# Kernel optimization log

Measured on AMD Instinct MI355X. Metric: run time of the kernel, lower is better.

The kernel has to match this reference:

```python
import jax, jax.numpy as jnp
import numpy as np

B, S = 128, 200
Q, K, V, C, SUM = 20000, 128, 128, 64, 128


def setup_inputs() -> dict:
    key = jax.random.key(0)
    ks = jax.random.split(key, 14)
    stdev = 1.0 / np.sqrt(C + K)  # NTM-style memory init bound

    def lin_w(k, fan_in, shape):
        b = 1.0 / np.sqrt(fan_in)
        return jax.random.uniform(k, shape, jnp.float32, -b, b)

    # embeddings with padding_idx=0 zeroed (PAD_INDEX=0)
    q_emb = jax.random.normal(ks[0], (Q + 1, K), jnp.float32).at[0].set(0.0)
    i_emb = jax.random.normal(ks[1], (2 * Q + 1, V), jnp.float32).at[0].set(0.0)
    key_memory = jax.random.uniform(ks[2], (K, C), jnp.float32, -stdev, stdev)
    init_value_memory = jax.random.uniform(ks[3], (V, C), jnp.float32, -stdev, stdev)
    erase_W = lin_w(ks[4], V, (V, V))
    erase_b = lin_w(ks[5], V, (V,))
    add_W = lin_w(ks[6], V, (V, V))
    add_b = lin_w(ks[7], V, (V,))
    summ_W = lin_w(ks[8], V + K, (V + K, SUM))
    summ_b = lin_w(ks[9], V + K, (SUM,))
    out_W = lin_w(ks[10], SUM, (SUM, 1))
    out_b = lin_w(ks[11], SUM, (1,))
    inp = jax.random.randint(ks[12], (B, S), 0, 2 * Q + 1)
    target_id = jax.random.randint(ks[13], (B,), 0, Q + 1)
    return dict(q_emb=q_emb, i_emb=i_emb, key_memory=key_memory,
                init_value_memory=init_value_memory,
                erase_W=erase_W, erase_b=erase_b, add_W=add_W, add_b=add_b,
                summ_W=summ_W, summ_b=summ_b, out_W=out_W, out_b=out_b,
                input=inp, target_id=target_id)


def reference(q_emb, i_emb, key_memory, init_value_memory,
              erase_W, erase_b, add_W, add_b,
              summ_W, summ_b, out_W, out_b,
              input, target_id):
    Qn = q_emb.shape[0] - 1
    bsz = input.shape[0]
    # map interaction index -> question id
    qid = input - Qn * (input > Qn).astype(input.dtype)          # (B,S)
    # all per-step quantities are independent of memory state -> precompute
    iv = i_emb[input]                                            # (B,S,V)
    e = jax.nn.sigmoid(iv @ erase_W + erase_b)                   # (B,S,V)
    a = jnp.tanh(iv @ add_W + add_b)                             # (B,S,V)
    w = jax.nn.softmax(q_emb[qid] @ key_memory, axis=-1)         # (B,S,C)

    mem0 = jnp.broadcast_to(init_value_memory, (bsz,) + init_value_memory.shape)  # (B,V,C)

    def step(mem, xs):
        e_t, a_t, w_t = xs                                       # (B,V),(B,V),(B,C)
        erase = e_t[:, :, None] * w_t[:, None, :]                # rank-1 outer, (B,V,C)
        add = a_t[:, :, None] * w_t[:, None, :]
        mem = mem * (1.0 - erase) + add
        return mem, None

    xs = (jnp.swapaxes(e, 0, 1), jnp.swapaxes(a, 0, 1), jnp.swapaxes(w, 0, 1))
    mem, _ = jax.lax.scan(step, mem0, xs)                        # (B,V,C)

    qv = q_emb[target_id]                                        # (B,K)
    wt = jax.nn.softmax(qv @ key_memory, axis=-1)                # (B,C)
    read = jnp.einsum('bvc,bc->bv', mem, wt)                     # (B,V)
    summ = jnp.tanh(jnp.concatenate([read, qv], axis=-1) @ summ_W + summ_b)
    return summ @ out_W + out_b                                  # (B,1), pre-sigmoid
```

## Files before the change

kernel.cpp:

```cpp
#include <hip/hip_runtime.h>
#include <hip/hip_bf16.h>
#include <hip/hip_fp16.h>

#define B_ 128
#define S_ 200
#define QN_ 20000
#define V_ 128
#define K_ 128
#define C_ 64
#define SUM_ 128
#define NCH 8
#define CL 25
#define RW 32

using short8 = __attribute__((ext_vector_type(8))) short;
using f32x4  = __attribute__((ext_vector_type(4))) float;

__device__ __forceinline__ float fast_sigmoid(float x) { return 1.f / (1.f + __expf(-x)); }
__device__ __forceinline__ float fast_tanh(float x)    { return 1.f - 2.f / (__expf(2.f * x) + 1.f); }

template<bool BF>
__device__ __forceinline__ float ld(const void* p, long long i) {
    if (BF) return __bfloat162float(((const __hip_bfloat16*)p)[i]);
    return ((const float*)p)[i];
}

__device__ __forceinline__ unsigned short f2bf(float v) {
    __hip_bfloat16 h = __float2bfloat16(v);
    unsigned short u;
    __builtin_memcpy(&u, &h, 2);
    return u;
}

__device__ __forceinline__ int probe_flag_wave(const void* erase_b) {
    const unsigned* w = (const unsigned*)erase_b;
    const int lane = threadIdx.x & 63;
    const unsigned lo = w[lane] & 0xffffu;
    const float f = __uint_as_float(lo << 16);
    const unsigned long long bal = __ballot(!(fabsf(f) <= 0.5f));
    return (__popcll(bal) <= 8) ? 1 : 0;
}

struct FusedLDS {
    unsigned short bufA[RW * 136];
    unsigned short bufB[RW * 136];
    float  wlog[RW * 68];
    int sidx[RW], sqid[RW];
};

template<bool BF>
__device__ __forceinline__ void fused_body(
    const void* q_emb, const void* i_emb,
    const void* erase_W, const void* add_W, const void* key_memory,
    const void* erase_b, const void* add_b,
    const int* __restrict__ input,
    __half* __restrict__ du, FusedLDS& sm)
{
    const int bid = blockIdx.x;
    const int b = bid & 127;
    const int chunk = bid >> 7;
    const int t = threadIdx.x;
    const int wv = t >> 6;
    const int lane = t & 63;
    const int lrow = lane & 15;
    const int lk8 = (lane >> 4) * 8;

    if (t < RW) {
        const int s = (t < CL) ? t : 0;
        const int ix = input[b * S_ + chunk * CL + s];
        sm.sidx[t] = ix;
        sm.sqid[t] = ix > QN_ ? ix - QN_ : ix;
    }
    __syncthreads();

    #pragma unroll
    for (int r = 0; r < 4; ++r) {
        const int j = t + 256 * r;
        const int tensor = j >> 9;
        const int row = (j >> 4) & 31;
        const int seg = j & 15;
        const int gr = tensor ? sm.sqid[row] : sm.sidx[row];
        unsigned short* dst = (tensor ? sm.bufB : sm.bufA) + row * 136 + seg * 8;
        if (BF) {
            const unsigned short* src = (const unsigned short*)(tensor ? q_emb : i_emb);
            *(uint4*)dst = *(const uint4*)(src + (long long)gr * 128 + seg * 8);
        } else {
            const float* src = (const float*)(tensor ? q_emb : i_emb) + (long long)gr * 128 + seg * 8;
            const float4 f0 = *(const float4*)src;
            const float4 f1 = *(const float4*)(src + 4);
            unsigned short o[8] = {f2bf(f0.x), f2bf(f0.y), f2bf(f0.z), f2bf(f0.w),
                                   f2bf(f1.x), f2bf(f1.y), f2bf(f1.z), f2bf(f1.w)};
            *(uint4*)dst = *(const uint4*)o;
        }
    }

    short8 bfr[5][4];
    int nco[5];
    float biasq[4];
    #pragma unroll
    for (int q = 0; q < 5; ++q) {
        const int nt = wv + 4 * q;
        const void* Wsrc;
        int ldn;
        if (q < 2)      { Wsrc = erase_W;    nco[q] = nt * 16 + lrow;        ldn = 128; }
        else if (q < 4) { Wsrc = add_W;      nco[q] = (nt - 8) * 16 + lrow;  ldn = 128; }
        else            { Wsrc = key_memory; nco[q] = (nt - 16) * 16 + lrow; ldn = 64; }
        if (q < 2)      biasq[q] = ld<BF>(erase_b, nco[q]);
        else if (q < 4) biasq[q] = ld<BF>(add_b, nco[q]);
        #pragma unroll
        for (int ks = 0; ks < 4; ++ks) {
            unsigned short o[8];
            #pragma unroll
            for (int jj = 0; jj < 8; ++jj) {
                const long long idx = (long long)(ks * 32 + lk8 + jj) * ldn + nco[q];
                o[jj] = f2bf(ld<BF>(Wsrc, idx));
            }
            bfr[q][ks] = *(const short8*)o;
        }
    }
    __syncthreads();

    __half* eshw = (__half*)sm.bufA;
    __half* ashw = (__half*)sm.bufB;
    #pragma unroll
    for (int mt = 0; mt < 2; ++mt) {
        short8 afr_iv[4], afr_qv[4];
        const unsigned short* arA = sm.bufA + (mt * 16 + lrow) * 136 + lk8;
        const unsigned short* arB = sm.bufB + (mt * 16 + lrow) * 136 + lk8;
        #pragma unroll
        for (int ks = 0; ks < 4; ++ks) {
            afr_iv[ks] = *(const short8*)(arA + ks * 32);
            afr_qv[ks] = *(const short8*)(arB + ks * 32);
        }
        __syncthreads();
        #pragma unroll
        for (int q = 0; q < 4; ++q) {
            f32x4 acc = {0.f, 0.f, 0.f, 0.f};
            #pragma unroll
            for (int ks = 0; ks < 4; ++ks)
                acc = __builtin_amdgcn_mfma_f32_16x16x32_bf16(afr_iv[ks], bfr[q][ks], acc, 0, 0, 0);
            const int ncol = nco[q];
            const float bb = biasq[q];
            #pragma unroll
            for (int r = 0; r < 4; ++r) {
                const int orow = mt * 16 + (lane >> 4) * 4 + r;
                const float y = acc[r] + bb;
                if (q < 2) eshw[orow * 136 + ncol] = __float2half(fast_sigmoid(y));
                else       ashw[orow * 136 + ncol] = __float2half(fast_tanh(y));
            }
        }
        {
            f32x4 acc = {0.f, 0.f, 0.f, 0.f};
            #pragma unroll
            for (int ks = 0; ks < 4; ++ks)
                acc = __builtin_amdgcn_mfma_f32_16x16x32_bf16(afr_qv[ks], bfr[4][ks], acc, 0, 0, 0);
            #pragma unroll
            for (int r = 0; r < 4; ++r)
                sm.wlog[(mt * 16 + (lane >> 4) * 4 + r) * 68 + nco[4]] = acc[r];
        }
    }
    __syncthreads();

    {
        const int row = t >> 3;
        const int cs = t & 7;
        float* wr = &sm.wlog[row * 68 + cs * 8];
        float v[8];
        *(float4*)&v[0] = *(const float4*)&wr[0];
        *(float4*)&v[4] = *(const float4*)&wr[4];
        float m = v[0];
        #pragma unroll
        for (int ii = 1; ii < 8; ++ii) m = fmaxf(m, v[ii]);
        m = fmaxf(m, __shfl_xor(m, 1, 64));
        m = fmaxf(m, __shfl_xor(m, 2, 64));
        m = fmaxf(m, __shfl_xor(m, 4, 64));
        float s = 0.f;
        #pragma unroll
        for (int ii = 0; ii < 8; ++ii) { v[ii] = __expf(v[ii] - m); s += v[ii]; }
        s += __shfl_xor(s, 1, 64);
        s += __shfl_xor(s, 2, 64);
        s += __shfl_xor(s, 4, 64);
        const float inv = 1.f / s;
        *(float4*)&wr[0] = make_float4(v[0]*inv, v[1]*inv, v[2]*inv, v[3]*inv);
        *(float4*)&wr[4] = make_float4(v[4]*inv, v[5]*inv, v[6]*inv, v[7]*inv);
    }
    __syncthreads();

    const int vg = t >> 3;
    const int cg = t & 7;
    const int v0 = vg * 4, c0 = cg * 8;
    const __half* esh = (const __half*)sm.bufA;
    const __half* ash = (const __half*)sm.bufB;

    const __half2 one2 = __floats2half2_rn(1.f, 1.f);
    const __half2 zero2 = __floats2half2_rn(0.f, 0.f);
    __half2 Dm2[4][4], Um2[4][4];
    #pragma unroll
    for (int i = 0; i < 4; ++i)
        #pragma unroll
        for (int jp = 0; jp < 4; ++jp) { Dm2[i][jp] = one2; Um2[i][jp] = zero2; }

    for (int s = 0; s < CL; ++s) {
        const __half2 e01 = *(const __half2*)(esh + s * 136 + v0);
        const __half2 e23 = *(const __half2*)(esh + s * 136 + v0 + 2);
        const __half2 a01 = *(const __half2*)(ash + s * 136 + v0);
        const __half2 a23 = *(const __half2*)(ash + s * 136 + v0 + 2);
        const float4 wf0 = *(const float4*)(sm.wlog + s * 68 + c0);
        const float4 wf1 = *(const float4*)(sm.wlog + s * 68 + c0 + 4);
        const __half2 w2[4] = { __floats2half2_rn(wf0.x, wf0.y), __floats2half2_rn(wf0.z, wf0.w),
                                __floats2half2_rn(wf1.x, wf1.y), __floats2half2_rn(wf1.z, wf1.w) };
        const __half2 e2[4] = { __low2half2(e01), __high2half2(e01),
                                __low2half2(e23), __high2half2(e23) };
        const __half2 a2[4] = { __low2half2(a01), __high2half2(a01),
                                __low2half2(a23), __high2half2(a23) };
        #pragma unroll
        for (int i = 0; i < 4; ++i) {
            const __half2 ne = __hneg2(e2[i]);
            #pragma unroll
            for (int jp = 0; jp < 4; ++jp) {
                const __half2 d2 = __hfma2(ne, w2[jp], one2);
                Dm2[i][jp] = __hmul2(Dm2[i][jp], d2);
                Um2[i][jp] = __hfma2(d2, Um2[i][jp], __hmul2(a2[i], w2[jp]));
            }
        }
    }

    __half* dbase = du + ((size_t)(chunk * B_ + b) * (V_ * C_ * 2));
    #pragma unroll
    for (int i = 0; i < 4; ++i) {
        __half* dst = dbase + (size_t)(v0 + i) * (C_ * 2) + c0;
        *(uint4*)dst        = *(const uint4*)&Dm2[i][0];
        *(uint4*)(dst + C_) = *(const uint4*)&Um2[i][0];
    }
}

__global__ __launch_bounds__(256) void dkvmn_fused(
    const void* q_emb, const void* i_emb,
    const void* erase_W, const void* add_W, const void* key_memory,
    const void* erase_b, const void* add_b,
    const int* __restrict__ input,
    __half* __restrict__ du)
{
    __shared__ FusedLDS sm;
    if (probe_flag_wave(erase_b))
        fused_body<true>(q_emb, i_emb, erase_W, add_W, key_memory,
                         erase_b, add_b, input, du, sm);
    else
        fused_body<false>(q_emb, i_emb, erase_W, add_W, key_memory,
                          erase_b, add_b, input, du, sm);
}

template<bool BF>
__device__ __forceinline__ void foldfinal_body(
    const void* init_value_memory, const void* q_emb, const void* key_memory,
    const void* summ_W, const void* summ_b,
    const void* out_W, const void* out_b,
    const int* __restrict__ target_id,
    const __half* __restrict__ du,
    void* __restrict__ outp, float* wtl, float* readl, float* summl)
{
    const int b = blockIdx.x;
    const int t = threadIdx.x;
    const int cg = t & 7;
    const int c0 = cg * 8;

    if (t < 64) {
        const long long qrow = (long long)target_id[b] * K_;
        float logit = 0.f;
        #pragma unroll 8
        for (int i = 0; i < K_; ++i)
            logit += ld<BF>(q_emb, qrow + i) * ld<BF>(key_memory, i * C_ + t);
        float m = logit;
        for (int off = 32; off > 0; off >>= 1)
            m = fmaxf(m, __shfl_xor(m, off, 64));
        const float ex = __expf(logit - m);
        float ssum = ex;
        for (int off = 32; off > 0; off >>= 1)
            ssum += __shfl_xor(ssum, off, 64);
        wtl[t] = ex / ssum;
    }
    __syncthreads();

    float wt8[8];
    *(float4*)&wt8[0] = *(const float4*)(wtl + c0);
    *(float4*)&wt8[4] = *(const float4*)(wtl + c0 + 4);

    #pragma unroll
    for (int sub = 0; sub < 4; ++sub) {
        const int v = sub * 32 + (t >> 3);

        uint4 qa[NCH], qb[NCH];
        #pragma unroll
        for (int ch = 0; ch < NCH; ++ch) {
            const __half* base = du + ((size_t)(ch * B_ + b) * (V_ * C_ * 2))
                                    + (size_t)v * (C_ * 2) + c0;
            qa[ch] = *(const uint4*)base;
            qb[ch] = *(const uint4*)(base + C_);
        }

        float mem[8];
        #pragma unroll
        for (int k = 0; k < 8; ++k)
            mem[k] = ld<BF>(init_value_memory, v * C_ + c0 + k);

        #pragma unroll
        for (int ch = 0; ch < NCH; ++ch) {
            const __half2* hD = (const __half2*)&qa[ch];
            const __half2* hU = (const __half2*)&qb[ch];
            #pragma unroll
            for (int k = 0; k < 4; ++k) {
                const float2 fD = __half22float2(hD[k]);
                const float2 fU = __half22float2(hU[k]);
                mem[2 * k]     = fmaf(fD.x, mem[2 * k],     fU.x);
                mem[2 * k + 1] = fmaf(fD.y, mem[2 * k + 1], fU.y);
            }
        }

        float pacc = 0.f;
        #pragma unroll
        for (int k = 0; k < 8; ++k) pacc += mem[k] * wt8[k];
        pacc += __shfl_xor(pacc, 1, 64);
        pacc += __shfl_xor(pacc, 2, 64);
        pacc += __shfl_xor(pacc, 4, 64);
        if (cg == 0) readl[v] = pacc;
    }
    __syncthreads();

    if (t < SUM_) {
        const long long qrow = (long long)target_id[b] * K_;
        float acc = ld<BF>(summ_b, t);
        #pragma unroll 8
        for (int i = 0; i < 128; ++i)
            acc += readl[i] * ld<BF>(summ_W, i * SUM_ + t);
        #pragma unroll 8
        for (int i = 0; i < 128; ++i)
            acc += ld<BF>(q_emb, qrow + i) * ld<BF>(summ_W, (128 + i) * SUM_ + t);
        summl[t] = fast_tanh(acc);
    }
    __syncthreads();

    if (t < 64) {
        float oacc = summl[t] * ld<BF>(out_W, t) + summl[t + 64] * ld<BF>(out_W, t + 64);
        for (int off = 32; off > 0; off >>= 1)
            oacc += __shfl_xor(oacc, off, 64);
        if (t == 0) {
            const float res = oacc + ld<BF>(out_b, 0);
            if (BF) ((__hip_bfloat16*)outp)[b] = __float2bfloat16(res);
            else    ((float*)outp)[b] = res;
        }
    }
}

__global__ __launch_bounds__(256) void dkvmn_foldfinal(
    const void* init_value_memory, const void* q_emb, const void* key_memory,
    const void* summ_W, const void* summ_b,
    const void* out_W, const void* out_b, const void* erase_b,
    const int* __restrict__ target_id,
    const __half* __restrict__ du,
    void* __restrict__ outp)
{
    __shared__ float wtl[C_], readl[V_], summl[SUM_];
    if (probe_flag_wave(erase_b))
        foldfinal_body<true>(init_value_memory, q_emb, key_memory, summ_W, summ_b,
                             out_W, out_b, target_id, du, outp, wtl, readl, summl);
    else
        foldfinal_body<false>(init_value_memory, q_emb, key_memory, summ_W, summ_b,
                              out_W, out_b, target_id, du, outp, wtl, readl, summl);
}

extern "C" void kernel_launch(void* const* d_in, const int* in_sizes, int n_in,
                              void* d_out, int out_size, void* d_ws, size_t ws_size,
                              hipStream_t stream) {
    const void* q_emb             = d_in[0];
    const void* i_emb             = d_in[1];
    const void* key_memory        = d_in[2];
    const void* init_value_memory = d_in[3];
    const void* erase_W           = d_in[4];
    const void* erase_b           = d_in[5];
    const void* add_W             = d_in[6];
    const void* add_b             = d_in[7];
    const void* summ_W            = d_in[8];
    const void* summ_b            = d_in[9];
    const void* out_W             = d_in[10];
    const void* out_b             = d_in[11];
    const int* input     = (const int*)d_in[12];
    const int* target_id = (const int*)d_in[13];

    __half* du = (__half*)d_ws;

    dkvmn_fused<<<NCH * B_, 256, 0, stream>>>(
        q_emb, i_emb, erase_W, add_W, key_memory, erase_b, add_b, input, du);
    dkvmn_foldfinal<<<B_, 256, 0, stream>>>(
        init_value_memory, q_emb, key_memory, summ_W, summ_b, out_W, out_b,
        erase_b, target_id, du, d_out);
}
```

Baseline: 166.4 us.

## Prepack bf16 MFMA weight fragments in a separate kernel and read them directly

Adds a small prepack kernel that converts erase_W, add_W and key_memory into bf16 MFMA B-fragment layout once per call, stored in workspace. The fused kernel no longer gathers scattered strided weight elements and converts them in each of the 1024 blocks. It instead loads contiguous 16-byte fragments at MFMA time, which frees the 20 short8 registers per thread that held the fragments. It also adds a launch_bounds occupancy hint of 4 blocks per CU. The cost is an extra kernel launch and repeated global/L2 reads of the packed weights inside the MFMA loop.

```diff
diff --git a/kernel.cpp b/kernel.cpp
--- a/kernel.cpp
+++ b/kernel.cpp
@@ -41,6 +41,41 @@
     return (__popcll(bal) <= 8) ? 1 : 0;
 }
 
+template<bool BF>
+__device__ __forceinline__ void prepack_body(
+    const void* erase_W, const void* add_W, const void* key_memory,
+    unsigned short* __restrict__ wpack)
+{
+    const int fid = blockIdx.x * 256 + threadIdx.x;
+    if (fid >= 5120) return;
+    const int lane = fid & 63;
+    const int ks = (fid >> 6) & 3;
+    const int wv = (fid >> 8) & 3;
+    const int q  = fid >> 10;
+    const int nt = wv + 4 * q;
+    const void* Wsrc;
+    int ncol, ldn;
+    if (q < 2)      { Wsrc = erase_W;    ncol = nt * 16 + (lane & 15);        ldn = 128; }
+    else if (q < 4) { Wsrc = add_W;      ncol = (nt - 8) * 16 + (lane & 15);  ldn = 128; }
+    else            { Wsrc = key_memory; ncol = (nt - 16) * 16 + (lane & 15); ldn = 64; }
+    const int k8 = (lane >> 4) * 8;
+    unsigned short o[8];
+    #pragma unroll
+    for (int jj = 0; jj < 8; ++jj) {
+        const long long idx = (long long)(ks * 32 + k8 + jj) * ldn + ncol;
+        o[jj] = f2bf(ld<BF>(Wsrc, idx));
+    }
+    *(uint4*)(wpack + (size_t)fid * 8) = *(const uint4*)o;
+}
+
+__global__ __launch_bounds__(256) void dkvmn_prepack(
+    const void* erase_W, const void* add_W, const void* key_memory,
+    const void* erase_b, unsigned short* __restrict__ wpack)
+{
+    if (probe_flag_wave(erase_b)) prepack_body<true >(erase_W, add_W, key_memory, wpack);
+    else                          prepack_body<false>(erase_W, add_W, key_memory, wpack);
+}
+
 struct FusedLDS {
     unsigned short bufA[RW * 136];
     unsigned short bufB[RW * 136];
@@ -51,9 +86,9 @@
 template<bool BF>
 __device__ __forceinline__ void fused_body(
     const void* q_emb, const void* i_emb,
-    const void* erase_W, const void* add_W, const void* key_memory,
     const void* erase_b, const void* add_b,
     const int* __restrict__ input,
+    const unsigned short* __restrict__ wpack,
     __half* __restrict__ du, FusedLDS& sm)
 {
     const int bid = blockIdx.x;
@@ -94,29 +129,16 @@
         }
     }
 
-    short8 bfr[5][4];
     int nco[5];
     float biasq[4];
     #pragma unroll
     for (int q = 0; q < 5; ++q) {
         const int nt = wv + 4 * q;
-        const void* Wsrc;
-        int ldn;
-        if (q < 2)      { Wsrc = erase_W;    nco[q] = nt * 16 + lrow;        ldn = 128; }
-        else if (q < 4) { Wsrc = add_W;      nco[q] = (nt - 8) * 16 + lrow;  ldn = 128; }
-        else            { Wsrc = key_memory; nco[q] = (nt - 16) * 16 + lrow; ldn = 64; }
+        if (q < 2)      nco[q] = nt * 16 + lrow;
+        else if (q < 4) nco[q] = (nt - 8) * 16 + lrow;
+        else            nco[q] = (nt - 16) * 16 + lrow;
         if (q < 2)      biasq[q] = ld<BF>(erase_b, nco[q]);
         else if (q < 4) biasq[q] = ld<BF>(add_b, nco[q]);
-        #pragma unroll
-        for (int ks = 0; ks < 4; ++ks) {
-            unsigned short o[8];
-            #pragma unroll
-            for (int jj = 0; jj < 8; ++jj) {
-                const long long idx = (long long)(ks * 32 + lk8 + jj) * ldn + nco[q];
-                o[jj] = f2bf(ld<BF>(Wsrc, idx));
-            }
-            bfr[q][ks] = *(const short8*)o;
-        }
     }
     __syncthreads();
 
@@ -137,8 +159,11 @@
         for (int q = 0; q < 4; ++q) {
             f32x4 acc = {0.f, 0.f, 0.f, 0.f};
             #pragma unroll
-            for (int ks = 0; ks < 4; ++ks)
-                acc = __builtin_amdgcn_mfma_f32_16x16x32_bf16(afr_iv[ks], bfr[q][ks], acc, 0, 0, 0);
+            for (int ks = 0; ks < 4; ++ks) {
+                const short8 bf = *(const short8*)(wpack +
+                    ((size_t)(((q * 4 + wv) * 4 + ks) * 64 + lane)) * 8);
+                acc = __builtin_amdgcn_mfma_f32_16x16x32_bf16(afr_iv[ks], bf, acc, 0, 0, 0);
+            }
             const int ncol = nco[q];
             const float bb = biasq[q];
             #pragma unroll
@@ -152,8 +177,11 @@
         {
             f32x4 acc = {0.f, 0.f, 0.f, 0.f};
             #pragma unroll
-            for (int ks = 0; ks < 4; ++ks)
-                acc = __builtin_amdgcn_mfma_f32_16x16x32_bf16(afr_qv[ks], bfr[4][ks], acc, 0, 0, 0);
+            for (int ks = 0; ks < 4; ++ks) {
+                const short8 bf = *(const short8*)(wpack +
+                    ((size_t)(((4 * 4 + wv) * 4 + ks) * 64 + lane)) * 8);
+                acc = __builtin_amdgcn_mfma_f32_16x16x32_bf16(afr_qv[ks], bf, acc, 0, 0, 0);
+            }
             #pragma unroll
             for (int r = 0; r < 4; ++r)
                 sm.wlog[(mt * 16 + (lane >> 4) * 4 + r) * 68 + nco[4]] = acc[r];
@@ -234,20 +262,18 @@
     }
 }
 
-__global__ __launch_bounds__(256) void dkvmn_fused(
+__global__ __launch_bounds__(256, 4) void dkvmn_fused(
     const void* q_emb, const void* i_emb,
-    const void* erase_W, const void* add_W, const void* key_memory,
     const void* erase_b, const void* add_b,
     const int* __restrict__ input,
+    const unsigned short* __restrict__ wpack,
     __half* __restrict__ du)
 {
     __shared__ FusedLDS sm;
     if (probe_flag_wave(erase_b))
-        fused_body<true>(q_emb, i_emb, erase_W, add_W, key_memory,
-                         erase_b, add_b, input, du, sm);
+        fused_body<true>(q_emb, i_emb, erase_b, add_b, input, wpack, du, sm);
     else
-        fused_body<false>(q_emb, i_emb, erase_W, add_W, key_memory,
-                          erase_b, add_b, input, du, sm);
+        fused_body<false>(q_emb, i_emb, erase_b, add_b, input, wpack, du, sm);
 }
 
 template<bool BF>
@@ -386,10 +412,13 @@
     const int* input     = (const int*)d_in[12];
     const int* target_id = (const int*)d_in[13];
 
-    __half* du = (__half*)d_ws;
-
+    unsigned short* wpack = (unsigned short*)d_ws;
+    __half* du = (__half*)(wpack + 5120 * 8);
+
+    dkvmn_prepack<<<20, 256, 0, stream>>>(
+        erase_W, add_W, key_memory, erase_b, wpack);
     dkvmn_fused<<<NCH * B_, 256, 0, stream>>>(
-        q_emb, i_emb, erase_W, add_W, key_memory, erase_b, add_b, input, du);
+        q_emb, i_emb, erase_b, add_b, input, wpack, du);
     dkvmn_foldfinal<<<B_, 256, 0, stream>>>(
         init_value_memory, q_emb, key_memory, summ_W, summ_b, out_W, out_b,
         erase_b, target_id, du, d_out);
```

After: 142.4 us. -14.4%, faster.
